# Kernel optimization log

Measured on AMD Instinct MI355X. Metric: run time of the kernel, lower is better.

Reference implementation:

```python
import jax, jax.numpy as jnp
import numpy as np

V, D, C, H = 32, 128, 2048, 8
B, M = 8, 2048
HD = D // H


def rms_norm(x, scale):
    # Whole-tensor (per-batch) RMS over dims (1,2), as in the source (quirky but faithful).
    Bx, Mx, Dx = x.shape
    fr = jnp.sqrt(jnp.sum(x * x, axis=(1, 2))) * (Mx * Dx) ** -0.5  # (B,)
    raw = x / fr[:, None, None]
    return scale[:Mx, :][None, :, :] * raw


def rope_tables(Mx):
    i = jnp.arange(D // 2, dtype=jnp.float32)
    # NOTE: faithful to source: exponent uses (i-1), not i.
    base = jnp.power(10000.0, -2.0 * (i - 1.0) / D)  # (D/2,)
    pos = jnp.arange(Mx, dtype=jnp.float32)
    ang = pos[:, None] * base[None, :]  # (M, D/2)
    return jnp.cos(ang), jnp.sin(ang)


def apply_rope(t, cos, sin):
    # Equivalent to bmm with the block-diagonal 2x2 rotation matrices:
    # out[2i]   =  t[2i]*cos + t[2i+1]*sin
    # out[2i+1] = -t[2i]*sin + t[2i+1]*cos
    te, to = t[..., 0::2], t[..., 1::2]
    oe = te * cos + to * sin
    oo = -te * sin + to * cos
    return jnp.stack([oe, oo], axis=-1).reshape(t.shape)


def mha(q, k, v, in_w, in_b, out_w, out_b):
    Bx, Mx, _ = q.shape
    qp = q @ in_w[:D].T + in_b[:D]
    kp = k @ in_w[D:2 * D].T + in_b[D:2 * D]
    vp = v @ in_w[2 * D:].T + in_b[2 * D:]
    qh = qp.reshape(Bx, Mx, H, HD).transpose(0, 2, 1, 3)
    kh = kp.reshape(Bx, Mx, H, HD).transpose(0, 2, 1, 3)
    vh = vp.reshape(Bx, Mx, H, HD).transpose(0, 2, 1, 3)
    scores = jnp.einsum('bhqd,bhkd->bhqk', qh, kh) / jnp.sqrt(jnp.float32(HD))
    causal = jnp.tril(jnp.ones((Mx, Mx), dtype=bool))
    scores = jnp.where(causal[None, None], scores, -jnp.inf)
    probs = jax.nn.softmax(scores, axis=-1)  # dropout=0.1 in train mode; eval here
    o = jnp.einsum('bhqk,bhkd->bhqd', probs, vh)
    o = o.transpose(0, 2, 1, 3).reshape(Bx, Mx, D)
    return o @ out_w.T + out_b


def setup_inputs():
    key = jax.random.key(0)
    ks = jax.random.split(key, 12)
    s = 0.02
    return {
        'idx': jax.random.randint(ks[0], (B, M), 0, V),
        'targets': jax.random.randint(ks[1], (B, M), 0, V),
        'emb': jax.random.normal(ks[2], (V, D), jnp.float32) * s,
        'rms_scale': jnp.ones((C, D), jnp.float32),
        'Wq': jax.random.normal(ks[3], (D, D), jnp.float32) * s,
        'Wk': jax.random.normal(ks[4], (D, D), jnp.float32) * s,
        'Wv': jax.random.normal(ks[5], (D, D), jnp.float32) * s,
        'in_proj_w': jax.random.normal(ks[6], (3 * D, D), jnp.float32) * s,
        'in_proj_b': jnp.zeros((3 * D,), jnp.float32),
        'out_proj_w': jax.random.normal(ks[7], (D, D), jnp.float32) * s,
        'out_proj_b': jnp.zeros((D,), jnp.float32),
        'lin_w': jax.random.normal(ks[8], (D, D), jnp.float32) * s,
        'lin_b': jnp.zeros((D,), jnp.float32),
        'out_w': jax.random.normal(ks[9], (V, D), jnp.float32) * s,
        'out_b': jnp.zeros((V,), jnp.float32),
    }


def reference(idx, targets, emb, rms_scale, Wq, Wk, Wv, in_proj_w, in_proj_b,
              out_proj_w, out_proj_b, lin_w, lin_b, out_w, out_b):
    x = emb[idx]                                  # (B, M, D)
    x = rms_norm(x, rms_scale)
    Q = x @ Wq.T
    K = x @ Wk.T
    Vv = x @ Wv.T
    cos, sin = rope_tables(x.shape[1])
    q_out = apply_rope(Q, cos, sin)
    k_out = apply_rope(K, cos, sin)
    v_out = apply_rope(Vv, cos, sin)              # source rotates V too (faithful)
    x = x + mha(q_out, k_out, v_out, in_proj_w, in_proj_b, out_proj_w, out_proj_b)
    x = rms_norm(x, rms_scale)
    x = x + jax.nn.relu(x @ lin_w.T + lin_b)
    logits = x @ out_w.T + out_b                  # (B, M, V)
    logp = jax.nn.log_softmax(logits, axis=-1)
    nll = -jnp.take_along_axis(logp, targets[..., None], axis=-1)[..., 0]
    loss = jnp.mean(nll)
    return logits, loss
```

## Files before the change

### kernel.cpp

```cpp
#include <hip/hip_runtime.h>
#include <hip/hip_bf16.h>
#include <math.h>

#define Vv   32
#define Dd   128
#define Hh   8
#define Bb   8
#define Mm   2048
#define BM   (Bb*Mm)
#define XNS  140
#define QKS  396

typedef _Float16 half4_t __attribute__((ext_vector_type(4)));
typedef _Float16 half8_t __attribute__((ext_vector_type(8)));
typedef __fp16   fp16x2  __attribute__((ext_vector_type(2)));
typedef float    float4_t __attribute__((ext_vector_type(4)));
#define MFMA16 __builtin_amdgcn_mfma_f32_16x16x16f16
#define MFMA32 __builtin_amdgcn_mfma_f32_16x16x32_f16

#if __has_builtin(__builtin_amdgcn_exp2f)
__device__ __forceinline__ float fexp2(float x) { return __builtin_amdgcn_exp2f(x); }
#else
__device__ __forceinline__ float fexp2(float x) { return __expf(x * 0.6931471805599453f); }
#endif

__global__ __launch_bounds__(256) void front_kernel(const float* __restrict__ Wq,
                                                    const float* __restrict__ Wk,
                                                    const float* __restrict__ Wv,
                                                    const float* __restrict__ in_w,
                                                    const float* __restrict__ out_pw,
                                                    const float* __restrict__ lin_w,
                                                    const float* __restrict__ out_w,
                                                    _Float16* __restrict__ Wh,
                                                    float* __restrict__ cosT,
                                                    float* __restrict__ sinT,
                                                    const int* __restrict__ idx,
                                                    const float* __restrict__ emb,
                                                    float* __restrict__ partials,
                                                    float* __restrict__ lossOut) {
    if (blockIdx.x < 1040) {
        if (blockIdx.x == 0 && threadIdx.x == 0) lossOut[0] = 0.f;
        int gid = blockIdx.x * 256 + threadIdx.x;
        if (gid < 135168) {
            const float* src;
            int i;
            if (gid < 131072) {
                int seg = gid >> 14; i = gid & 16383;
                src = seg == 0 ? Wq : seg == 1 ? Wk : seg == 2 ? Wv :
                      seg < 6 ? in_w + (size_t)(seg - 3) * 16384 :
                      seg == 6 ? out_pw : lin_w;
            } else { src = out_w; i = gid - 131072; }
            int tile = i >> 8, within = i & 255;
            int nt = tile >> 3, kk = tile & 7;
            int r = within >> 4, cc = within & 15;
            Wh[gid] = (_Float16)src[(nt * 16 + r) * 128 + kk * 16 + cc];
        } else {
            int rid = gid - 135168;
            int i = rid & 63, m = rid >> 6;
            float ex = -2.0f * ((float)i - 1.0f) / 128.0f;
            float basef = expf(ex * 9.210340371976184f);
            float ang = (float)m * basef;
            cosT[rid] = cosf(ang);
            sinT[rid] = sinf(ang);
        }
    } else {
        int b = blockIdx.x - 1040;
        __shared__ int   hc[4][32];
        __shared__ float n2[32];
        int tid = threadIdx.x;
        int wave = tid >> 6;
        if (tid < 128) ((int*)hc)[tid] = 0;
        __syncthreads();
        const int* ib = idx + b * Mm;
        #pragma unroll
        for (int k = 0; k < 8; k++) atomicAdd(&hc[wave][ib[tid * 8 + k]], 1);
        {
            int v = tid >> 3, part = tid & 7;
            const float* ep = emb + v * 128 + part * 16;
            float s = 0.f;
            #pragma unroll
            for (int q = 0; q < 4; q++) {
                float4 x = *(const float4*)(ep + q * 4);
                s += x.x * x.x + x.y * x.y + x.z * x.z + x.w * x.w;
            }
            s += __shfl_xor(s, 1); s += __shfl_xor(s, 2); s += __shfl_xor(s, 4);
            if (part == 0) n2[v] = s;
        }
        __syncthreads();
        if (tid < 32) {
            int cnt = ((hc[0][tid] + hc[1][tid]) + (hc[2][tid] + hc[3][tid]));
            float t = (float)cnt * n2[tid];
            #pragma unroll
            for (int off = 16; off; off >>= 1) t += __shfl_xor(t, off);
            if (tid == 0) partials[b] = t;
        }
    }
}

__global__ __launch_bounds__(512, 4) void gemm_qkvproj_kernel(const int* __restrict__ idx,
                                                              const float* __restrict__ emb,
                                                              const float* __restrict__ scale,
                                                              const float* __restrict__ part1,
                                                              const _Float16* __restrict__ Whqkv,
                                                              const _Float16* __restrict__ Whin,
                                                              const float* __restrict__ in_b,
                                                              const float* __restrict__ cosT,
                                                              const float* __restrict__ sinT,
                                                              _Float16* __restrict__ xnh,
                                                              _Float16* __restrict__ Qp,
                                                              _Float16* __restrict__ Kp,
                                                              _Float16* __restrict__ Vp) {
    __shared__ _Float16 xn[32 * XNS];
    __shared__ _Float16 qkv[32 * QKS];
    int tid = threadIdx.x;
    int row0 = blockIdx.x * 32;
    float iv = 512.0f / sqrtf(part1[row0 >> 11]);
    {
        int rw = tid >> 4, c8 = (tid & 15) * 8;
        int m = (row0 + rw) & (Mm - 1);
        const float* ep = emb + (size_t)idx[row0 + rw] * 128 + c8;
        float4 xa = *(const float4*)ep;
        float4 xb = *(const float4*)(ep + 4);
        const float* sp = scale + (size_t)m * 128 + c8;
        float4 s0 = *(const float4*)sp;
        float4 s1 = *(const float4*)(sp + 4);
        half8_t o8;
        o8[0] = (_Float16)(xa.x * iv * s0.x);
        o8[1] = (_Float16)(xa.y * iv * s0.y);
        o8[2] = (_Float16)(xa.z * iv * s0.z);
        o8[3] = (_Float16)(xa.w * iv * s0.w);
        o8[4] = (_Float16)(xb.x * iv * s1.x);
        o8[5] = (_Float16)(xb.y * iv * s1.y);
        o8[6] = (_Float16)(xb.z * iv * s1.z);
        o8[7] = (_Float16)(xb.w * iv * s1.w);
        *(half8_t*)(xn + rw * XNS + c8) = o8;
        *(half8_t*)(xnh + (size_t)(row0 + rw) * 128 + c8) = o8;
    }
    __syncthreads();
    int wave = tid >> 6, lane = tid & 63;
    int r = lane & 15, c = lane >> 4;
    int nb = wave * 48;
    int aoff = c * 8;
    int boff = r * 16 + (c & 1) * 8;
    int bsel = c >> 1;
    {
        float4_t acc[2][3];
        #pragma unroll
        for (int rt = 0; rt < 2; rt++)
            #pragma unroll
            for (int t = 0; t < 3; t++) acc[rt][t] = (float4_t){0.f, 0.f, 0.f, 0.f};
        #pragma unroll
        for (int kk = 0; kk < 4; kk++) {
            half8_t a0 = *(const half8_t*)(xn + r * XNS + kk * 32 + aoff);
            half8_t a1 = *(const half8_t*)(xn + (16 + r) * XNS + kk * 32 + aoff);
            half8_t wf[3];
            #pragma unroll
            for (int t = 0; t < 3; t++)
                wf[t] = *(const half8_t*)(Whqkv + ((wave * 3 + t) * 8 + kk * 2 + bsel) * 256 + boff);
            #pragma unroll
            for (int t = 0; t < 3; t++) {
                acc[0][t] = MFMA32(a0, wf[t], acc[0][t], 0, 0, 0);
                acc[1][t] = MFMA32(a1, wf[t], acc[1][t], 0, 0, 0);
            }
        }
        #pragma unroll
        for (int rt = 0; rt < 2; rt++) {
            #pragma unroll
            for (int t = 0; t < 3; t++) {
                int n = nb + t * 16 + r;
                int ci = (n & 127) >> 1;
                #pragma unroll
                for (int reg = 0; reg < 4; reg++) {
                    int m2 = (row0 + rt * 16 + 4 * c + reg) & (Mm - 1);
                    float v = acc[rt][t][reg];
                    float vp = __shfl_xor(v, 1);
                    float cs = cosT[m2 * 64 + ci], sn = sinT[m2 * 64 + ci];
                    v = (n & 1) ? (-vp * sn + v * cs) : (v * cs + vp * sn);
                    qkv[(rt * 16 + 4 * c + reg) * QKS + n] = (_Float16)v;
                }
            }
        }
    }
    __syncthreads();
    {
        int seg_lo = nb >> 7;
        int seg_hi = (nb + 32) >> 7;
        float4_t acc[2][3];
        #pragma unroll
        for (int rt = 0; rt < 2; rt++)
            #pragma unroll
            for (int t = 0; t < 3; t++) acc[rt][t] = (float4_t){0.f, 0.f, 0.f, 0.f};
        #pragma unroll
        for (int kk = 0; kk < 4; kk++) {
            half8_t al0 = *(const half8_t*)(qkv + r * QKS + seg_lo * 128 + kk * 32 + aoff);
            half8_t al1 = *(const half8_t*)(qkv + (16 + r) * QKS + seg_lo * 128 + kk * 32 + aoff);
            half8_t ah0 = *(const half8_t*)(qkv + r * QKS + seg_hi * 128 + kk * 32 + aoff);
            half8_t ah1 = *(const half8_t*)(qkv + (16 + r) * QKS + seg_hi * 128 + kk * 32 + aoff);
            #pragma unroll
            for (int t = 0; t < 3; t++) {
                int colg = nb + t * 16;
                int seg = colg >> 7;
                int ntl = (colg & 127) >> 4;
                half8_t wf = *(const half8_t*)(Whin + ((seg * 8 + ntl) * 8 + kk * 2 + bsel) * 256 + boff);
                bool lo = (seg == seg_lo);
                acc[0][t] = MFMA32(lo ? al0 : ah0, wf, acc[0][t], 0, 0, 0);
                acc[1][t] = MFMA32(lo ? al1 : ah1, wf, acc[1][t], 0, 0, 0);
            }
        }
        int bb = row0 >> 11;
        #pragma unroll
        for (int rt = 0; rt < 2; rt++) {
            int t16 = ((row0 + rt * 16) & 2047) >> 4;
            #pragma unroll
            for (int t = 0; t < 3; t++) {
                int colg = nb + t * 16;
                int seg = colg >> 7;
                int h = (colg & 127) >> 4;
                size_t tb = ((size_t)(bb * 8 + h) * 128 + t16) * 256;
                float bv = in_b[colg + r];
                _Float16* dst = seg == 0 ? Qp : seg == 1 ? Kp : Vp;
                #pragma unroll
                for (int reg = 0; reg < 4; reg++) {
                    float v = acc[rt][t][reg] + bv;
                    int key = 4 * c + reg;
                    if (seg < 2) dst[tb + key * 16 + r] = (_Float16)v;
                    else         dst[tb + r * 16 + key] = (_Float16)v;
                }
            }
        }
    }
}

__global__ __launch_bounds__(512, 4) void gemm_ep1_kernel(const _Float16* __restrict__ Oh,
                                                          const _Float16* __restrict__ W6,
                                                          const float* __restrict__ bias,
                                                          const _Float16* __restrict__ xnh,
                                                          _Float16* __restrict__ xresh,
                                                          float* __restrict__ partials) {
    __shared__ _Float16 At[32 * XNS];
    int tid = threadIdx.x;
    int row0 = blockIdx.x * 32;
    {
        int rw = tid >> 4, c8 = (tid & 15) * 8;
        *(half8_t*)(At + rw * XNS + c8) = *(const half8_t*)(Oh + (size_t)(row0 + rw) * 128 + c8);
    }
    __syncthreads();
    int wave = tid >> 6, lane = tid & 63;
    int r = lane & 15, c = lane >> 4;
    int aoff = c * 8;
    int boff = r * 16 + (c & 1) * 8;
    int bsel = c >> 1;
    int n0 = wave * 16;
    float4_t acc[2];
    acc[0] = (float4_t){0.f, 0.f, 0.f, 0.f};
    acc[1] = (float4_t){0.f, 0.f, 0.f, 0.f};
    #pragma unroll
    for (int kk = 0; kk < 4; kk++) {
        half8_t a0 = *(const half8_t*)(At + r * XNS + kk * 32 + aoff);
        half8_t a1 = *(const half8_t*)(At + (16 + r) * XNS + kk * 32 + aoff);
        half8_t wf = *(const half8_t*)(W6 + (wave * 8 + kk * 2 + bsel) * 256 + boff);
        acc[0] = MFMA32(a0, wf, acc[0], 0, 0, 0);
        acc[1] = MFMA32(a1, wf, acc[1], 0, 0, 0);
    }
    float lssq = 0.f;
    int n = n0 + r;
    float bv = bias[n];
    #pragma unroll
    for (int rt = 0; rt < 2; rt++) {
        #pragma unroll
        for (int reg = 0; reg < 4; reg++) {
            int row = row0 + rt * 16 + 4 * c + reg;
            float v = acc[rt][reg] + bv + (float)xnh[(size_t)row * 128 + n];
            lssq += v * v;
            xresh[(size_t)row * 128 + n] = (_Float16)v;
        }
    }
    #pragma unroll
    for (int off = 32; off; off >>= 1) lssq += __shfl_xor(lssq, off);
    __shared__ float wsum[8];
    if (lane == 0) wsum[wave] = lssq;
    __syncthreads();
    if (tid == 0) partials[blockIdx.x] = ((wsum[0] + wsum[1]) + (wsum[2] + wsum[3])) +
                                        ((wsum[4] + wsum[5]) + (wsum[6] + wsum[7]));
}

__global__ __launch_bounds__(512, 4) void gemm_ep2_logits_kernel(const _Float16* __restrict__ xresh,
                                                                 const float* __restrict__ scale,
                                                                 const float* __restrict__ part2,
                                                                 const _Float16* __restrict__ W7,
                                                                 const float* __restrict__ bias,
                                                                 const _Float16* __restrict__ Wo16,
                                                                 const float* __restrict__ bo,
                                                                 const int* __restrict__ targets,
                                                                 float* __restrict__ logits,
                                                                 float* __restrict__ lossOut) {
    __shared__ _Float16 At[32 * XNS];
    __shared__ _Float16 Ao[32 * XNS];
    __shared__ float wn[2];
    int tid = threadIdx.x;
    int row0 = blockIdx.x * 32;
    float pv = part2[(row0 >> 11) * 64 + (tid & 63)];
    #pragma unroll
    for (int off = 32; off; off >>= 1) pv += __shfl_xor(pv, off);
    float iv = 512.0f / sqrtf(pv);
    {
        int rw = tid >> 4, c8 = (tid & 15) * 8;
        int m = (row0 + rw) & (Mm - 1);
        half8_t x8 = *(const half8_t*)(xresh + (size_t)(row0 + rw) * 128 + c8);
        const float* sp = scale + (size_t)m * 128 + c8;
        float4 s0 = *(const float4*)sp;
        float4 s1 = *(const float4*)(sp + 4);
        half8_t o8;
        o8[0] = (_Float16)((float)x8[0] * iv * s0.x);
        o8[1] = (_Float16)((float)x8[1] * iv * s0.y);
        o8[2] = (_Float16)((float)x8[2] * iv * s0.z);
        o8[3] = (_Float16)((float)x8[3] * iv * s0.w);
        o8[4] = (_Float16)((float)x8[4] * iv * s1.x);
        o8[5] = (_Float16)((float)x8[5] * iv * s1.y);
        o8[6] = (_Float16)((float)x8[6] * iv * s1.z);
        o8[7] = (_Float16)((float)x8[7] * iv * s1.w);
        *(half8_t*)(At + rw * XNS + c8) = o8;
    }
    __syncthreads();
    int wave = tid >> 6, lane = tid & 63;
    int r = lane & 15, c = lane >> 4;
    int aoff = c * 8;
    int boff = r * 16 + (c & 1) * 8;
    int bsel = c >> 1;
    int n0 = wave * 16;
    float4_t acc[2];
    acc[0] = (float4_t){0.f, 0.f, 0.f, 0.f};
    acc[1] = (float4_t){0.f, 0.f, 0.f, 0.f};
    #pragma unroll
    for (int kk = 0; kk < 4; kk++) {
        half8_t a0 = *(const half8_t*)(At + r * XNS + kk * 32 + aoff);
        half8_t a1 = *(const half8_t*)(At + (16 + r) * XNS + kk * 32 + aoff);
        half8_t wf = *(const half8_t*)(W7 + (wave * 8 + kk * 2 + bsel) * 256 + boff);
        acc[0] = MFMA32(a0, wf, acc[0], 0, 0, 0);
        acc[1] = MFMA32(a1, wf, acc[1], 0, 0, 0);
    }
    int n = n0 + r;
    float bv = bias[n];
    #pragma unroll
    for (int rt = 0; rt < 2; rt++) {
        #pragma unroll
        for (int reg = 0; reg < 4; reg++) {
            int row = row0 + rt * 16 + 4 * c + reg;
            int rowl = rt * 16 + 4 * c + reg;
            float v = fmaxf(acc[rt][reg] + bv, 0.f) + (float)xresh[(size_t)row * 128 + n];
            Ao[rowl * XNS + n] = (_Float16)v;
        }
    }
    __syncthreads();
    if (wave < 2) {
        int rloc = wave * 16;
        half8_t lf[4];
        #pragma unroll
        for (int kk = 0; kk < 4; kk++)
            lf[kk] = *(const half8_t*)(Ao + (rloc + r) * XNS + kk * 32 + aoff);
        float4_t lacc[2];
        lacc[0] = (float4_t){0.f, 0.f, 0.f, 0.f};
        lacc[1] = (float4_t){0.f, 0.f, 0.f, 0.f};
        #pragma unroll
        for (int kk = 0; kk < 4; kk++) {
            #pragma unroll
            for (int t = 0; t < 2; t++) {
                half8_t wf = *(const half8_t*)(Wo16 + (t * 8 + kk * 2 + bsel) * 256 + boff);
                lacc[t] = MFMA32(lf[kk], wf, lacc[t], 0, 0, 0);
            }
        }
        float b0 = bo[r], b1 = bo[r + 16];
        float nll_s = 0.f;
        #pragma unroll
        for (int reg = 0; reg < 4; reg++) {
            int row = row0 + rloc + 4 * c + reg;
            float l0 = lacc[0][reg] + b0;
            float l1 = lacc[1][reg] + b1;
            logits[(size_t)row * 32 + r] = l0;
            logits[(size_t)row * 32 + 16 + r] = l1;
            float mx = fmaxf(l0, l1);
            #pragma unroll
            for (int off = 8; off; off >>= 1) mx = fmaxf(mx, __shfl_xor(mx, off));
            float se = __expf(l0 - mx) + __expf(l1 - mx);
            #pragma unroll
            for (int off = 8; off; off >>= 1) se += __shfl_xor(se, off);
            int tgt = targets[row];
            float sel = (tgt & 16) ? l1 : l0;
            float tval = __shfl(sel, (lane & 48) | (tgt & 15));
            nll_s += logf(se) + mx - tval;
        }
        nll_s += __shfl_xor(nll_s, 16);
        nll_s += __shfl_xor(nll_s, 32);
        if (lane == 0) wn[wave] = nll_s;
    }
    __syncthreads();
    if (tid == 0) atomicAdd(lossOut, (wn[0] + wn[1]) * (1.0f / (float)BM));
}

__device__ __forceinline__ half4_t attn_exps(float4_t st, float& ls) {
    float p0 = fexp2(st[0]), p1 = fexp2(st[1]);
    float p2 = fexp2(st[2]), p3 = fexp2(st[3]);
    ls += (p0 + p1) + (p2 + p3);
    fp16x2 lo = __builtin_amdgcn_cvt_pkrtz(p0, p1);
    fp16x2 hi = __builtin_amdgcn_cvt_pkrtz(p2, p3);
    half4_t pf;
    pf[0] = (_Float16)lo[0]; pf[1] = (_Float16)lo[1];
    pf[2] = (_Float16)hi[0]; pf[3] = (_Float16)hi[1];
    return pf;
}
__device__ __forceinline__ half4_t attn_exps_masked(float4_t st, float& ls, int r, int c) {
    float p0 = (4 * c + 0 <= r) ? fexp2(st[0]) : 0.f;
    float p1 = (4 * c + 1 <= r) ? fexp2(st[1]) : 0.f;
    float p2 = (4 * c + 2 <= r) ? fexp2(st[2]) : 0.f;
    float p3 = (4 * c + 3 <= r) ? fexp2(st[3]) : 0.f;
    ls += (p0 + p1) + (p2 + p3);
    fp16x2 lo = __builtin_amdgcn_cvt_pkrtz(p0, p1);
    fp16x2 hi = __builtin_amdgcn_cvt_pkrtz(p2, p3);
    half4_t pf;
    pf[0] = (_Float16)lo[0]; pf[1] = (_Float16)lo[1];
    pf[2] = (_Float16)hi[0]; pf[3] = (_Float16)hi[1];
    return pf;
}

__global__ __launch_bounds__(256) void attn_kernel(const _Float16* __restrict__ Qp,
                                                   const _Float16* __restrict__ Kp,
                                                   const _Float16* __restrict__ Vp,
                                                   _Float16* __restrict__ Oh) {
    __shared__ float mrg[2][10][64];
    int wave = threadIdx.x >> 6, lane = threadIdx.x & 63;
    int pair = blockIdx.x * 2 + (wave >> 1);
    int split = wave & 1;
    int qa = pair & 63, bh = pair >> 6, qb = 127 - qa;
    int r = lane & 15, c = lane >> 4;
    int lofs = r * 16 + 4 * c;
    const _Float16* Kb = Kp + (size_t)bh * 32768 + lofs;
    const _Float16* Vb = Vp + (size_t)bh * 32768 + lofs;
    const _Float16* Qb = Qp + (size_t)bh * 32768 + lofs;
    half4_t qfa = *(const half4_t*)(Qb + qa * 256);
    half4_t qfb = *(const half4_t*)(Qb + qb * 256);
    const _Float16 qscale = (_Float16)0.36067376f;
    qfa *= qscale;
    qfb *= qscale;
    float4_t zero = {0.f, 0.f, 0.f, 0.f};
    float4_t oa = zero, ob = zero;
    float lsa = 0.f, lsb = 0.f;

    for (int kt = split; kt < qa; kt += 2) {
        half4_t k0 = *(const half4_t*)(Kb + (size_t)kt * 256);
        half4_t v0 = *(const half4_t*)(Vb + (size_t)kt * 256);
        float4_t sa = MFMA16(k0, qfa, zero, 0, 0, 0);
        float4_t sb = MFMA16(k0, qfb, zero, 0, 0, 0);
        half4_t pa = attn_exps(sa, lsa);
        half4_t pb = attn_exps(sb, lsb);
        oa = MFMA16(pa, v0, oa, 0, 0, 0);
        ob = MFMA16(pb, v0, ob, 0, 0, 0);
    }
    if ((qa & 1) == split) {
        half4_t k0 = *(const half4_t*)(Kb + (size_t)qa * 256);
        half4_t v0 = *(const half4_t*)(Vb + (size_t)qa * 256);
        float4_t sa = MFMA16(k0, qfa, zero, 0, 0, 0);
        float4_t sb = MFMA16(k0, qfb, zero, 0, 0, 0);
        half4_t pa = attn_exps_masked(sa, lsa, r, c);
        half4_t pb = attn_exps(sb, lsb);
        oa = MFMA16(pa, v0, oa, 0, 0, 0);
        ob = MFMA16(pb, v0, ob, 0, 0, 0);
    }
    {
        int s = qa + 1;
        if ((s & 1) != split) s++;
        for (int kt = s; kt < qb; kt += 2) {
            half4_t k0 = *(const half4_t*)(Kb + (size_t)kt * 256);
            half4_t v0 = *(const half4_t*)(Vb + (size_t)kt * 256);
            float4_t sb = MFMA16(k0, qfb, zero, 0, 0, 0);
            half4_t pb = attn_exps(sb, lsb);
            ob = MFMA16(pb, v0, ob, 0, 0, 0);
        }
    }
    if ((qb & 1) == split) {
        half4_t k0 = *(const half4_t*)(Kb + (size_t)qb * 256);
        half4_t v0 = *(const half4_t*)(Vb + (size_t)qb * 256);
        float4_t sb = MFMA16(k0, qfb, zero, 0, 0, 0);
        half4_t pb = attn_exps_masked(sb, lsb, r, c);
        ob = MFMA16(pb, v0, ob, 0, 0, 0);
    }
    int pib = wave >> 1;
    if (split == 1) {
        #pragma unroll
        for (int i = 0; i < 4; i++) {
            mrg[pib][i][lane] = oa[i];
            mrg[pib][4 + i][lane] = ob[i];
        }
        mrg[pib][8][lane] = lsa;
        mrg[pib][9][lane] = lsb;
    }
    __syncthreads();
    if (split == 0) {
        #pragma unroll
        for (int i = 0; i < 4; i++) {
            oa[i] += mrg[pib][i][lane];
            ob[i] += mrg[pib][4 + i][lane];
        }
        lsa += mrg[pib][8][lane];
        lsb += mrg[pib][9][lane];
        lsa += __shfl_xor(lsa, 16); lsa += __shfl_xor(lsa, 32);
        lsb += __shfl_xor(lsb, 16); lsb += __shfl_xor(lsb, 32);
        int b = bh >> 3, h = bh & 7;
        #pragma unroll
        for (int reg = 0; reg < 4; reg++) {
            float la = __shfl(lsa, 4 * c + reg);
            float lb = __shfl(lsb, 4 * c + reg);
            Oh[(size_t)(b * Mm + qa * 16 + 4 * c + reg) * 128 + h * 16 + r] = (_Float16)(oa[reg] / la);
            Oh[(size_t)(b * Mm + qb * 16 + 4 * c + reg) * 128 + h * 16 + r] = (_Float16)(ob[reg] / lb);
        }
    }
}

extern "C" void kernel_launch(void* const* d_in, const int* in_sizes, int n_in,
                              void* d_out, int out_size, void* d_ws, size_t ws_size,
                              hipStream_t stream) {
    const int*   idx       = (const int*)d_in[0];
    const int*   targets   = (const int*)d_in[1];
    const float* emb       = (const float*)d_in[2];
    const float* rms_scale = (const float*)d_in[3];
    const float* Wq        = (const float*)d_in[4];
    const float* Wk        = (const float*)d_in[5];
    const float* Wv        = (const float*)d_in[6];
    const float* in_w      = (const float*)d_in[7];
    const float* in_b      = (const float*)d_in[8];
    const float* out_pw    = (const float*)d_in[9];
    const float* out_pb    = (const float*)d_in[10];
    const float* lin_w     = (const float*)d_in[11];
    const float* lin_b     = (const float*)d_in[12];
    const float* out_w     = (const float*)d_in[13];
    const float* out_b     = (const float*)d_in[14];
    float* out = (float*)d_out;
    float* lossOut = out + (size_t)BM * Vv;

    char* base = (char*)d_ws;
    const size_t MB = 1024 * 1024;
    _Float16* xnh   = (_Float16*)(base + 4 * MB);
    _Float16* Oh    = (_Float16*)(base + 8 * MB);
    _Float16* xresh = (_Float16*)(base + 12 * MB);
    _Float16* Qp    = (_Float16*)(base + 20 * MB);
    _Float16* Kp    = (_Float16*)(base + 24 * MB);
    _Float16* Vp    = (_Float16*)(base + 28 * MB);
    float*    cosT  = (float*)(base + 32 * MB);
    float*    sinT  = cosT + Mm * 64;
    float*    part1 = sinT + Mm * 64;
    float*    part2 = part1 + 2048;
    _Float16* Wh    = (_Float16*)(part2 + 512);

    front_kernel<<<1040 + 8, 256, 0, stream>>>(Wq, Wk, Wv, in_w, out_pw, lin_w, out_w,
                                               Wh, cosT, sinT, idx, emb, part1, lossOut);

    gemm_qkvproj_kernel<<<BM / 32, 512, 0, stream>>>(idx, emb, rms_scale, part1,
                                                     Wh, Wh + 3 * 16384, in_b,
                                                     cosT, sinT, xnh, Qp, Kp, Vp);

    attn_kernel<<<4096 / 2, 256, 0, stream>>>(Qp, Kp, Vp, Oh);

    gemm_ep1_kernel<<<BM / 32, 512, 0, stream>>>(Oh, Wh + 6 * 16384, out_pb, xnh, xresh, part2);

    gemm_ep2_logits_kernel<<<BM / 32, 512, 0, stream>>>(xresh, rms_scale, part2,
                                                        Wh + 7 * 16384, lin_b,
                                                        Wh + 131072, out_b, targets,
                                                        out, lossOut);
}
```

Measured before the change: 151.6 us.

## Stage K/V tiles in shared memory for attention kernel block

```diff
diff --git a/kernel.cpp b/kernel.cpp
--- a/kernel.cpp
+++ b/kernel.cpp
@@ -426,82 +426,112 @@
                                                    const _Float16* __restrict__ Kp,
                                                    const _Float16* __restrict__ Vp,
                                                    _Float16* __restrict__ Oh) {
-    __shared__ float mrg[2][10][64];
-    int wave = threadIdx.x >> 6, lane = threadIdx.x & 63;
-    int pair = blockIdx.x * 2 + (wave >> 1);
-    int split = wave & 1;
-    int qa = pair & 63, bh = pair >> 6, qb = 127 - qa;
+    __shared__ __align__(16) _Float16 Kl[16 * 256];
+    __shared__ __align__(16) _Float16 Vl[16 * 256];
+    float (*mrg)[10][64] = (float (*)[10][64])Kl;
+    int tid = threadIdx.x;
+    int wave = tid >> 6, lane = tid & 63;
+    int pi = wave >> 1, split = wave & 1;
+    int blk2 = blockIdx.x * 2;
+    int qa0 = blk2 & 63;
+    int bh = blk2 >> 6;
+    int qaw = qa0 + pi;
+    int qbw = 127 - qaw;
+    int maxk = 127 - qa0;
     int r = lane & 15, c = lane >> 4;
-    int lofs = r * 16 + 4 * c;
-    const _Float16* Kb = Kp + (size_t)bh * 32768 + lofs;
-    const _Float16* Vb = Vp + (size_t)bh * 32768 + lofs;
-    const _Float16* Qb = Qp + (size_t)bh * 32768 + lofs;
-    half4_t qfa = *(const half4_t*)(Qb + qa * 256);
-    half4_t qfb = *(const half4_t*)(Qb + qb * 256);
+    const _Float16* Kg = Kp + (size_t)bh * 32768;
+    const _Float16* Vg = Vp + (size_t)bh * 32768;
+    const _Float16* Qb = Qp + (size_t)bh * 32768 + r * 16 + 4 * c;
+    half4_t qfa = *(const half4_t*)(Qb + qaw * 256);
+    half4_t qfb = *(const half4_t*)(Qb + qbw * 256);
     const _Float16 qscale = (_Float16)0.36067376f;
     qfa *= qscale;
     qfb *= qscale;
     float4_t zero = {0.f, 0.f, 0.f, 0.f};
     float4_t oa = zero, ob = zero;
     float lsa = 0.f, lsb = 0.f;
-
-    for (int kt = split; kt < qa; kt += 2) {
-        half4_t k0 = *(const half4_t*)(Kb + (size_t)kt * 256);
-        half4_t v0 = *(const half4_t*)(Vb + (size_t)kt * 256);
-        float4_t sa = MFMA16(k0, qfa, zero, 0, 0, 0);
-        float4_t sb = MFMA16(k0, qfb, zero, 0, 0, 0);
-        half4_t pa = attn_exps(sa, lsa);
-        half4_t pb = attn_exps(sb, lsb);
-        oa = MFMA16(pa, v0, oa, 0, 0, 0);
-        ob = MFMA16(pb, v0, ob, 0, 0, 0);
-    }
-    if ((qa & 1) == split) {
-        half4_t k0 = *(const half4_t*)(Kb + (size_t)qa * 256);
-        half4_t v0 = *(const half4_t*)(Vb + (size_t)qa * 256);
-        float4_t sa = MFMA16(k0, qfa, zero, 0, 0, 0);
-        float4_t sb = MFMA16(k0, qfb, zero, 0, 0, 0);
-        half4_t pa = attn_exps_masked(sa, lsa, r, c);
-        half4_t pb = attn_exps(sb, lsb);
-        oa = MFMA16(pa, v0, oa, 0, 0, 0);
-        ob = MFMA16(pb, v0, ob, 0, 0, 0);
-    }
-    {
-        int s = qa + 1;
-        if ((s & 1) != split) s++;
-        for (int kt = s; kt < qb; kt += 2) {
-            half4_t k0 = *(const half4_t*)(Kb + (size_t)kt * 256);
-            half4_t v0 = *(const half4_t*)(Vb + (size_t)kt * 256);
+    int stile = tid >> 4;
+    int srr   = tid & 15;
+
+    for (int tb = 0; tb <= maxk; tb += 16) {
+        __syncthreads();
+        int kt = tb + stile;
+        if (kt <= maxk) {
+            const _Float16* kp8 = Kg + (size_t)kt * 256 + srr * 16;
+            const _Float16* vp8 = Vg + (size_t)kt * 256 + srr * 16;
+            half8_t klo = *(const half8_t*)kp8;
+            half8_t khi = *(const half8_t*)(kp8 + 8);
+            half8_t vlo = *(const half8_t*)vp8;
+            half8_t vhi = *(const half8_t*)(vp8 + 8);
+            _Float16* dk = Kl + stile * 256;
+            _Float16* dv = Vl + stile * 256;
+            half4_t t0, t1, t2, t3;
+            t0[0]=klo[0]; t0[1]=klo[1]; t0[2]=klo[2]; t0[3]=klo[3];
+            t1[0]=klo[4]; t1[1]=klo[5]; t1[2]=klo[6]; t1[3]=klo[7];
+            t2[0]=khi[0]; t2[1]=khi[1]; t2[2]=khi[2]; t2[3]=khi[3];
+            t3[0]=khi[4]; t3[1]=khi[5]; t3[2]=khi[6]; t3[3]=khi[7];
+            *(half4_t*)(dk + (srr +  0) * 4) = t0;
+            *(half4_t*)(dk + (srr + 16) * 4) = t1;
+            *(half4_t*)(dk + (srr + 32) * 4) = t2;
+            *(half4_t*)(dk + (srr + 48) * 4) = t3;
+            t0[0]=vlo[0]; t0[1]=vlo[1]; t0[2]=vlo[2]; t0[3]=vlo[3];
+            t1[0]=vlo[4]; t1[1]=vlo[5]; t1[2]=vlo[6]; t1[3]=vlo[7];
+            t2[0]=vhi[0]; t2[1]=vhi[1]; t2[2]=vhi[2]; t2[3]=vhi[3];
+            t3[0]=vhi[4]; t3[1]=vhi[5]; t3[2]=vhi[6]; t3[3]=vhi[7];
+            *(half4_t*)(dv + (srr +  0) * 4) = t0;
+            *(half4_t*)(dv + (srr + 16) * 4) = t1;
+            *(half4_t*)(dv + (srr + 32) * 4) = t2;
+            *(half4_t*)(dv + (srr + 48) * 4) = t3;
+        }
+        __syncthreads();
+        int jend = qbw - tb;
+        if (jend > 15) jend = 15;
+        for (int j = split; j <= jend; j += 2) {
+            int kt2 = tb + j;
+            half4_t k0 = *(const half4_t*)(Kl + j * 256 + lane * 4);
+            half4_t v0 = *(const half4_t*)(Vl + j * 256 + lane * 4);
             float4_t sb = MFMA16(k0, qfb, zero, 0, 0, 0);
-            half4_t pb = attn_exps(sb, lsb);
-            ob = MFMA16(pb, v0, ob, 0, 0, 0);
-        }
-    }
-    if ((qb & 1) == split) {
-        half4_t k0 = *(const half4_t*)(Kb + (size_t)qb * 256);
-        half4_t v0 = *(const half4_t*)(Vb + (size_t)qb * 256);
-        float4_t sb = MFMA16(k0, qfb, zero, 0, 0, 0);
-        half4_t pb = attn_exps_masked(sb, lsb, r, c);
-        ob = MFMA16(pb, v0, ob, 0, 0, 0);
-    }
-    int pib = wave >> 1;
+            if (kt2 < qaw) {
+                float4_t sa = MFMA16(k0, qfa, zero, 0, 0, 0);
+                half4_t pa = attn_exps(sa, lsa);
+                half4_t pb = attn_exps(sb, lsb);
+                oa = MFMA16(pa, v0, oa, 0, 0, 0);
+                ob = MFMA16(pb, v0, ob, 0, 0, 0);
+            } else if (kt2 == qaw) {
+                float4_t sa = MFMA16(k0, qfa, zero, 0, 0, 0);
+                half4_t pa = attn_exps_masked(sa, lsa, r, c);
+                half4_t pb = attn_exps(sb, lsb);
+                oa = MFMA16(pa, v0, oa, 0, 0, 0);
+                ob = MFMA16(pb, v0, ob, 0, 0, 0);
+            } else if (kt2 < qbw) {
+                half4_t pb = attn_exps(sb, lsb);
+                ob = MFMA16(pb, v0, ob, 0, 0, 0);
+            } else {
+                half4_t pb = attn_exps_masked(sb, lsb, r, c);
+                ob = MFMA16(pb, v0, ob, 0, 0, 0);
+            }
+        }
+    }
+
+    __syncthreads();
     if (split == 1) {
         #pragma unroll
         for (int i = 0; i < 4; i++) {
-            mrg[pib][i][lane] = oa[i];
-            mrg[pib][4 + i][lane] = ob[i];
-        }
-        mrg[pib][8][lane] = lsa;
-        mrg[pib][9][lane] = lsb;
+            mrg[pi][i][lane] = oa[i];
+            mrg[pi][4 + i][lane] = ob[i];
+        }
+        mrg[pi][8][lane] = lsa;
+        mrg[pi][9][lane] = lsb;
     }
     __syncthreads();
     if (split == 0) {
         #pragma unroll
         for (int i = 0; i < 4; i++) {
-            oa[i] += mrg[pib][i][lane];
-            ob[i] += mrg[pib][4 + i][lane];
-        }
-        lsa += mrg[pib][8][lane];
-        lsb += mrg[pib][9][lane];
+            oa[i] += mrg[pi][i][lane];
+            ob[i] += mrg[pi][4 + i][lane];
+        }
+        lsa += mrg[pi][8][lane];
+        lsb += mrg[pi][9][lane];
         lsa += __shfl_xor(lsa, 16); lsa += __shfl_xor(lsa, 32);
         lsb += __shfl_xor(lsb, 16); lsb += __shfl_xor(lsb, 32);
         int b = bh >> 3, h = bh & 7;
@@ -509,8 +539,8 @@
         for (int reg = 0; reg < 4; reg++) {
             float la = __shfl(lsa, 4 * c + reg);
             float lb = __shfl(lsb, 4 * c + reg);
-            Oh[(size_t)(b * Mm + qa * 16 + 4 * c + reg) * 128 + h * 16 + r] = (_Float16)(oa[reg] / la);
-            Oh[(size_t)(b * Mm + qb * 16 + 4 * c + reg) * 128 + h * 16 + r] = (_Float16)(ob[reg] / lb);
+            Oh[(size_t)(b * Mm + qaw * 16 + 4 * c + reg) * 128 + h * 16 + r] = (_Float16)(oa[reg] / la);
+            Oh[(size_t)(b * Mm + qbw * 16 + 4 * c + reg) * 128 + h * 16 + r] = (_Float16)(ob[reg] / lb);
         }
     }
 }
```

Result: no change. 152.3 us (+0.5%).
